# Kernel tuning notes

Hardware: AMD Instinct MI355X
Metric: run time of the kernel (lower is better)

Reference implementation:

```python
import jax, jax.numpy as jnp
import numpy as np

V, D = 100000, 128
B, Q, C, T = 1024, 64, 64, 8


def setup_inputs() -> dict:
    key = jax.random.key(0)
    ks = jax.random.split(key, 9)
    embed = jax.random.normal(ks[0], (V, D), dtype=jnp.float32) * 0.1
    embed = embed.at[0].set(0.0)  # padding_idx=0
    q_ids = jax.random.randint(ks[1], (B, Q), 1, V)
    c_ids = jax.random.randint(ks[2], (B, C, T), 1, V)
    num_qs = jax.random.randint(ks[3], (B,), 1, Q + 1)
    num_cols = jax.random.randint(ks[4], (B,), 1, C + 1)
    W_h = jax.random.normal(ks[5], (5 * D, D), dtype=jnp.float32) * 0.02
    b_h = jnp.zeros((D,), jnp.float32)
    W_o = jax.random.normal(ks[6], (D, 1), dtype=jnp.float32) * 0.02
    b_o = jnp.zeros((1,), jnp.float32)
    return {"q_ids": q_ids, "c_ids": c_ids, "num_qs": num_qs, "num_cols": num_cols,
            "embed": embed, "W_h": W_h, "b_h": b_h, "W_o": W_o, "b_o": b_o}


def _forward(q_ids, c_ids, num_qs, num_cols, embed, W_h, b_h, W_o, b_o):
    d = embed.shape[1]
    # ColumnSummarizer: pad-masked mean over column tokens -> [B, C, D]
    c_tok = embed[c_ids]                       # [B, C, T, D]
    c_mask = (c_ids != 0).astype(c_tok.dtype)  # [B, C, T]
    denom = jnp.maximum(c_mask.sum(-1, keepdims=True), 1.0)
    c_h = (c_tok * c_mask[..., None]).sum(-2) / denom  # [B, C, D]
    # QuestionSummarizer: q_h = token embeddings, q_summary = length-masked mean
    q_h = embed[q_ids]                         # [B, Q, D]
    q_valid = (jnp.arange(q_h.shape[1])[None, :] < num_qs[:, None])  # [B, Q]
    qv = q_valid.astype(q_h.dtype)
    q_summary = (q_h * qv[..., None]).sum(1) / jnp.maximum(
        num_qs[:, None].astype(q_h.dtype), 1.0)  # [B, D]
    # scaled dot-product attention, columns attend over question tokens
    sim = jnp.einsum('bcd,bqd->bcq', c_h, q_h) / jnp.sqrt(jnp.asarray(d, c_h.dtype))
    sim = jnp.where(q_valid[:, None, :], sim, -jnp.inf)  # mask padded q tokens
    att = jax.nn.softmax(sim, axis=-1)                    # [B, C, Q]
    weighted_q = jnp.einsum('bcq,bqd->bcd', att, q_h)     # [B, C, D]
    q_tiled = jnp.broadcast_to(q_summary[:, None, :], c_h.shape)
    feats = jnp.concatenate(
        [q_tiled, c_h, weighted_q, c_h * weighted_q, jnp.abs(c_h - weighted_q)],
        axis=-1)                                           # [B, C, 5D]
    h = jnp.tanh(feats @ W_h + b_h)
    return h @ W_o + b_o                                   # [B, C, 1]


def reference(q_ids, c_ids, num_qs, num_cols, embed, W_h, b_h, W_o, b_o):
    return _forward(q_ids, c_ids, num_qs, num_cols, embed, W_h, b_h, W_o, b_o)
```

## Files before the change

### kernel.cpp

```cpp
#include <hip/hip_runtime.h>


typedef __attribute__((ext_vector_type(8))) short     short8;
typedef __attribute__((ext_vector_type(8))) __bf16    bf16x8;
typedef __attribute__((ext_vector_type(4))) float     f32x4;

#define SWZ(row, off) ((off) ^ (((row) & 7) << 4))

#define CH_OFF    0
#define QH_OFF    16384
#define QHT_OFF   32768
#define ATT_OFF   49152
#define PROD_OFF  57344
#define QPART_OFF 73728
#define QSUM_OFF  77824
#define OUTP_OFF  78080
#define LDS_SIZE  79104

__device__ __forceinline__ unsigned short f2bf(float x) {
    unsigned u = __builtin_bit_cast(unsigned, x);
    u += 0x7FFFu + ((u >> 16) & 1u);
    return (unsigned short)(u >> 16);
}
__device__ __forceinline__ float bf2f(unsigned short u) {
    return __builtin_bit_cast(float, ((unsigned)u) << 16);
}
__device__ __forceinline__ f32x4 mfma16(short8 a, short8 b, f32x4 c) {
    return __builtin_amdgcn_mfma_f32_16x16x32_bf16(
        __builtin_bit_cast(bf16x8, a), __builtin_bit_cast(bf16x8, b), c, 0, 0, 0);
}

__global__ __launch_bounds__(256) void el_prep(const float* __restrict__ W_h,
                                               unsigned short* __restrict__ whT) {
    int t = blockIdx.x * 256 + threadIdx.x;
    int k = t >> 7, n = t & 127;
    whT[n * 640 + k] = f2bf(W_h[t]);
}

__global__ __launch_bounds__(256) void el_main(
    const int* __restrict__ q_ids, const int* __restrict__ c_ids,
    const int* __restrict__ num_qs, const float* __restrict__ embed,
    const unsigned short* __restrict__ whT, const float* __restrict__ b_h,
    const float* __restrict__ W_o, const float* __restrict__ b_o,
    float* __restrict__ out)
{
    __shared__ __align__(16) char smem[LDS_SIZE];
    const int tid = threadIdx.x;
    const int b = blockIdx.x;
    const int nq = num_qs[b];

    {
        const int l = tid & 31, g = tid >> 5;
        for (int c = g; c < 64; c += 8) {
            const int* cid = c_ids + ((b << 6) + c) * 8;
            f32x4 acc = {0.f, 0.f, 0.f, 0.f};
            int cnt = 0;
            #pragma unroll
            for (int t = 0; t < 8; ++t) {
                int id = cid[t];
                cnt += (id != 0);
                f32x4 v = *(const f32x4*)(embed + (long)id * 128 + l * 4);
                acc += v;
            }
            float inv = 1.0f / (float)(cnt > 0 ? cnt : 1);
            unsigned u01 = (unsigned)f2bf(acc[0] * inv) | ((unsigned)f2bf(acc[1] * inv) << 16);
            unsigned u23 = (unsigned)f2bf(acc[2] * inv) | ((unsigned)f2bf(acc[3] * inv) << 16);
            uint2 pk; pk.x = u01; pk.y = u23;
            *(uint2*)(smem + CH_OFF + SWZ(c, c * 256 + l * 8)) = pk;
        }
        f32x4 qacc = {0.f, 0.f, 0.f, 0.f};
        for (int q = g; q < 64; q += 8) {
            int id = q_ids[(b << 6) + q];
            f32x4 v = *(const f32x4*)(embed + (long)id * 128 + l * 4);
            unsigned u01 = (unsigned)f2bf(v[0]) | ((unsigned)f2bf(v[1]) << 16);
            unsigned u23 = (unsigned)f2bf(v[2]) | ((unsigned)f2bf(v[3]) << 16);
            uint2 pk; pk.x = u01; pk.y = u23;
            *(uint2*)(smem + QH_OFF + SWZ(q, q * 256 + l * 8)) = pk;
            #pragma unroll
            for (int i = 0; i < 4; ++i) {
                int d = l * 4 + i;
                *(unsigned short*)(smem + QHT_OFF + SWZ(d, d * 128 + q * 2)) = f2bf(v[i]);
            }
            if (q < nq) qacc += v;
        }
        *(f32x4*)(smem + QPART_OFF + (g * 128 + l * 4) * 4) = qacc;
    }
    __syncthreads();

    if (tid < 128) {
        float s = 0.f;
        #pragma unroll
        for (int g = 0; g < 8; ++g)
            s += *(const float*)(smem + QPART_OFF + (g * 128 + tid) * 4);
        s /= (float)(nq > 0 ? nq : 1);
        *(unsigned short*)(smem + QSUM_OFF + tid * 2) = f2bf(s);
    }
    __syncthreads();

    const int lane = tid & 63, w = tid >> 6;
    const int lr = lane & 15, lg = lane >> 4;

    {
        short8 a[4];
        const int arow = w * 16 + lr;
        #pragma unroll
        for (int s = 0; s < 4; ++s)
            a[s] = *(const short8*)(smem + CH_OFF + SWZ(arow, arow * 256 + s * 64 + lg * 16));
        f32x4 sim[4];
        #pragma unroll
        for (int ct = 0; ct < 4; ++ct) {
            f32x4 acc = {0.f, 0.f, 0.f, 0.f};
            const int q = ct * 16 + lr;
            #pragma unroll
            for (int s = 0; s < 4; ++s) {
                short8 bf = *(const short8*)(smem + QH_OFF + SWZ(q, q * 256 + s * 64 + lg * 16));
                acc = mfma16(a[s], bf, acc);
            }
            sim[ct] = acc;
        }
        const float scale = 0.08838834764831845f;
        #pragma unroll
        for (int ct = 0; ct < 4; ++ct) {
            const int q = ct * 16 + lr;
            #pragma unroll
            for (int r = 0; r < 4; ++r)
                sim[ct][r] = (q < nq) ? sim[ct][r] * scale : -3.0e38f;
        }
        float mx[4], sm[4];
        #pragma unroll
        for (int r = 0; r < 4; ++r)
            mx[r] = fmaxf(fmaxf(sim[0][r], sim[1][r]), fmaxf(sim[2][r], sim[3][r]));
        #pragma unroll
        for (int off = 1; off <= 8; off <<= 1)
            #pragma unroll
            for (int r = 0; r < 4; ++r)
                mx[r] = fmaxf(mx[r], __shfl_xor(mx[r], off));
        #pragma unroll
        for (int ct = 0; ct < 4; ++ct)
            #pragma unroll
            for (int r = 0; r < 4; ++r)
                sim[ct][r] = __expf(sim[ct][r] - mx[r]);
        #pragma unroll
        for (int r = 0; r < 4; ++r)
            sm[r] = (sim[0][r] + sim[1][r]) + (sim[2][r] + sim[3][r]);
        #pragma unroll
        for (int off = 1; off <= 8; off <<= 1)
            #pragma unroll
            for (int r = 0; r < 4; ++r)
                sm[r] += __shfl_xor(sm[r], off);
        float inv[4];
        #pragma unroll
        for (int r = 0; r < 4; ++r) inv[r] = 1.0f / sm[r];
        const int cbase = w * 16 + lg * 4;
        #pragma unroll
        for (int ct = 0; ct < 4; ++ct)
            #pragma unroll
            for (int r = 0; r < 4; ++r) {
                int c = cbase + r, q = ct * 16 + lr;
                *(unsigned short*)(smem + ATT_OFF + SWZ(c, c * 128 + q * 2)) =
                    f2bf(sim[ct][r] * inv[r]);
            }
    }
    __syncthreads();

    f32x4 wqa[8];
    {
        short8 pa[2];
        const int prow = w * 16 + lr;
        #pragma unroll
        for (int s = 0; s < 2; ++s)
            pa[s] = *(const short8*)(smem + ATT_OFF + SWZ(prow, prow * 128 + s * 64 + lg * 16));
        #pragma unroll
        for (int ct = 0; ct < 8; ++ct) {
            f32x4 acc = {0.f, 0.f, 0.f, 0.f};
            const int dcol = ct * 16 + lr;
            #pragma unroll
            for (int s = 0; s < 2; ++s) {
                short8 bf = *(const short8*)(smem + QHT_OFF + SWZ(dcol, dcol * 128 + s * 64 + lg * 16));
                acc = mfma16(pa[s], bf, acc);
            }
            wqa[ct] = acc;
        }
    }
    __syncthreads();
    {
        const int cbase = w * 16 + lg * 4;
        #pragma unroll
        for (int ct = 0; ct < 8; ++ct)
            #pragma unroll
            for (int r = 0; r < 4; ++r) {
                int c = cbase + r, d = ct * 16 + lr;
                int off = c * 256 + d * 2;
                float wqv = wqa[ct][r];
                float chv = bf2f(*(const unsigned short*)(smem + CH_OFF + SWZ(c, off)));
                *(unsigned short*)(smem + QH_OFF  + SWZ(c, off)) = f2bf(wqv);
                *(unsigned short*)(smem + PROD_OFF + SWZ(c, off)) = f2bf(chv * wqv);
                *(unsigned short*)(smem + QHT_OFF + SWZ(c, off)) = f2bf(fabsf(chv - wqv));
            }
    }
    __syncthreads();

    {
        f32x4 acc[4][2];
        #pragma unroll
        for (int rt = 0; rt < 4; ++rt)
            #pragma unroll
            for (int j = 0; j < 2; ++j)
                acc[rt][j] = (f32x4){0.f, 0.f, 0.f, 0.f};

        const int n0 = (w * 2) * 16 + lr;
        const int n1 = (w * 2 + 1) * 16 + lr;
        const int klane = lg * 8;
        short8 b0 = *(const short8*)(whT + n0 * 640 + klane);
        short8 b1 = *(const short8*)(whT + n1 * 640 + klane);

        for (int s = 0; s < 20; ++s) {
            short8 nb0 = b0, nb1 = b1;
            if (s < 19) {
                nb0 = *(const short8*)(whT + n0 * 640 + (s + 1) * 32 + klane);
                nb1 = *(const short8*)(whT + n1 * 640 + (s + 1) * 32 + klane);
            }
            const int p = s >> 2, sk = (s & 3) * 32;
            if (p == 0) {
                short8 afr = *(const short8*)(smem + QSUM_OFF + sk * 2 + lg * 16);
                #pragma unroll
                for (int rt = 0; rt < 4; ++rt) {
                    acc[rt][0] = mfma16(afr, b0, acc[rt][0]);
                    acc[rt][1] = mfma16(afr, b1, acc[rt][1]);
                }
            } else {
                const int base = (p == 1) ? CH_OFF : (p == 2) ? QH_OFF
                               : (p == 3) ? PROD_OFF : QHT_OFF;
                #pragma unroll
                for (int rt = 0; rt < 4; ++rt) {
                    int row = rt * 16 + lr;
                    short8 afr = *(const short8*)(smem + base + SWZ(row, row * 256 + sk * 2 + lg * 16));
                    acc[rt][0] = mfma16(afr, b0, acc[rt][0]);
                    acc[rt][1] = mfma16(afr, b1, acc[rt][1]);
                }
            }
            b0 = nb0; b1 = nb1;
        }

        float bh0 = b_h[n0], bh1 = b_h[n1];
        float wo0 = W_o[n0], wo1 = W_o[n1];
        #pragma unroll
        for (int rt = 0; rt < 4; ++rt)
            #pragma unroll
            for (int r = 0; r < 4; ++r) {
                float x0 = acc[rt][0][r] + bh0;
                float x1 = acc[rt][1][r] + bh1;
                float t0 = 1.0f - 2.0f / (__expf(2.0f * x0) + 1.0f);
                float t1 = 1.0f - 2.0f / (__expf(2.0f * x1) + 1.0f);
                float po = t0 * wo0 + t1 * wo1;
                #pragma unroll
                for (int off = 1; off <= 8; off <<= 1)
                    po += __shfl_xor(po, off);
                if (lr == 0)
                    *(float*)(smem + OUTP_OFF + (w * 64 + rt * 16 + lg * 4 + r) * 4) = po;
            }
    }
    __syncthreads();

    if (tid < 64) {
        float o = b_o[0];
        #pragma unroll
        for (int w2 = 0; w2 < 4; ++w2)
            o += *(const float*)(smem + OUTP_OFF + (w2 * 64 + tid) * 4);
        out[(b << 6) + tid] = o;
    }
}

extern "C" void kernel_launch(void* const* d_in, const int* in_sizes, int n_in,
                              void* d_out, int out_size, void* d_ws, size_t ws_size,
                              hipStream_t stream) {
    const int*   q_ids  = (const int*)d_in[0];
    const int*   c_ids  = (const int*)d_in[1];
    const int*   num_qs = (const int*)d_in[2];
    const float* embed  = (const float*)d_in[4];
    const float* W_h    = (const float*)d_in[5];
    const float* b_h    = (const float*)d_in[6];
    const float* W_o    = (const float*)d_in[7];
    const float* b_o    = (const float*)d_in[8];
    float*       out    = (float*)d_out;
    unsigned short* whT = (unsigned short*)d_ws;

    el_prep<<<320, 256, 0, stream>>>(W_h, whT);
    el_main<<<1024, 256, 0, stream>>>(q_ids, c_ids, num_qs, embed, whT,
                                      b_h, W_o, b_o, out);
}
```

Before: 171.3 us.

## Gather from a bf16 embedding copy, shrink LDS, fuse feature products into GEMM

Each call now converts the whole embedding table to bf16 in a separate pass, and the main kernel gathers column and question tokens from that copy. This halves the bytes moved by the random row gathers, at the cost of a full-table read and write per call. The LDS layout is compacted and buffers are reused so more blocks can fit per CU, and the launch bound now asks for three. The product and absolute-difference features are computed in registers inside the hidden-layer MFMA loop instead of being stored to LDS. The question transpose and the question summary are rebuilt from LDS, and token ids are staged in shared memory first.

```diff
diff --git a/kernel.cpp b/kernel.cpp
--- a/kernel.cpp
+++ b/kernel.cpp
@@ -10,12 +10,13 @@
 #define CH_OFF    0
 #define QH_OFF    16384
 #define QHT_OFF   32768
-#define ATT_OFF   49152
-#define PROD_OFF  57344
-#define QPART_OFF 73728
-#define QSUM_OFF  77824
-#define OUTP_OFF  78080
-#define LDS_SIZE  79104
+#define X_OFF     49152
+#define IDS_C     (X_OFF)
+#define IDS_Q     (X_OFF + 2048)
+#define QSP_OFF   (X_OFF)
+#define QSUM_OFF  (X_OFF + 1024)
+#define OUTP_OFF  (X_OFF + 1280)
+#define LDS_SIZE  (X_OFF + 2304)
 
 __device__ __forceinline__ unsigned short f2bf(float x) {
     unsigned u = __builtin_bit_cast(unsigned, x);
@@ -24,6 +25,12 @@
 }
 __device__ __forceinline__ float bf2f(unsigned short u) {
     return __builtin_bit_cast(float, ((unsigned)u) << 16);
+}
+__device__ __forceinline__ float bflo(unsigned u) {
+    return __builtin_bit_cast(float, u << 16);
+}
+__device__ __forceinline__ float bfhi(unsigned u) {
+    return __builtin_bit_cast(float, u & 0xFFFF0000u);
 }
 __device__ __forceinline__ f32x4 mfma16(short8 a, short8 b, f32x4 c) {
     return __builtin_amdgcn_mfma_f32_16x16x32_bf16(
@@ -37,9 +44,24 @@
     whT[n * 640 + k] = f2bf(W_h[t]);
 }
 
-__global__ __launch_bounds__(256) void el_main(
+__global__ __launch_bounds__(256) void el_conv(const float* __restrict__ e,
+                                               unsigned short* __restrict__ ebf) {
+    long i = ((long)blockIdx.x * 256 + threadIdx.x) * 8;
+    f32x4 a = *(const f32x4*)(e + i);
+    f32x4 c = *(const f32x4*)(e + i + 4);
+    uint4 pk;
+    pk.x = (unsigned)f2bf(a[0]) | ((unsigned)f2bf(a[1]) << 16);
+    pk.y = (unsigned)f2bf(a[2]) | ((unsigned)f2bf(a[3]) << 16);
+    pk.z = (unsigned)f2bf(c[0]) | ((unsigned)f2bf(c[1]) << 16);
+    pk.w = (unsigned)f2bf(c[2]) | ((unsigned)f2bf(c[3]) << 16);
+    *(uint4*)(ebf + i) = pk;
+}
+
+template <bool BF16E>
+__global__ __launch_bounds__(256, 3) void el_main(
     const int* __restrict__ q_ids, const int* __restrict__ c_ids,
-    const int* __restrict__ num_qs, const float* __restrict__ embed,
+    const int* __restrict__ num_qs, const float* __restrict__ emb,
+    const unsigned short* __restrict__ ebf,
     const unsigned short* __restrict__ whT, const float* __restrict__ b_h,
     const float* __restrict__ W_o, const float* __restrict__ b_o,
     float* __restrict__ out)
@@ -47,59 +69,120 @@
     __shared__ __align__(16) char smem[LDS_SIZE];
     const int tid = threadIdx.x;
     const int b = blockIdx.x;
-    const int nq = num_qs[b];
-
-    {
+    const int nq = num_qs[b] > 0 ? num_qs[b] : 1;
+
+    {
+        int* idc = (int*)(smem + IDS_C);
+        idc[tid]       = c_ids[(b << 9) + tid];
+        idc[tid + 256] = c_ids[(b << 9) + tid + 256];
+        if (tid < 64) ((int*)(smem + IDS_Q))[tid] = q_ids[(b << 6) + tid];
+    }
+    __syncthreads();
+
+    if constexpr (BF16E) {
+        const int l4 = tid & 15, gg = tid >> 4;
+        #pragma unroll 2
+        for (int cc = 0; cc < 4; ++cc) {
+            const int c = gg + cc * 16;
+            const int* idp = (const int*)(smem + IDS_C) + c * 8;
+            int id8[8];
+            #pragma unroll
+            for (int t = 0; t < 8; ++t) id8[t] = idp[t];
+            float acc[8] = {0.f,0.f,0.f,0.f,0.f,0.f,0.f,0.f};
+            int cnt = 0;
+            #pragma unroll
+            for (int t = 0; t < 8; ++t) {
+                uint4 v = *(const uint4*)(ebf + (long)id8[t] * 128 + l4 * 8);
+                cnt += (id8[t] != 0);
+                acc[0] += bflo(v.x); acc[1] += bfhi(v.x);
+                acc[2] += bflo(v.y); acc[3] += bfhi(v.y);
+                acc[4] += bflo(v.z); acc[5] += bfhi(v.z);
+                acc[6] += bflo(v.w); acc[7] += bfhi(v.w);
+            }
+            float inv = 1.0f / (float)(cnt > 0 ? cnt : 1);
+            uint4 pk;
+            pk.x = (unsigned)f2bf(acc[0]*inv) | ((unsigned)f2bf(acc[1]*inv) << 16);
+            pk.y = (unsigned)f2bf(acc[2]*inv) | ((unsigned)f2bf(acc[3]*inv) << 16);
+            pk.z = (unsigned)f2bf(acc[4]*inv) | ((unsigned)f2bf(acc[5]*inv) << 16);
+            pk.w = (unsigned)f2bf(acc[6]*inv) | ((unsigned)f2bf(acc[7]*inv) << 16);
+            *(uint4*)(smem + CH_OFF + SWZ(c, c * 256 + l4 * 16)) = pk;
+        }
+        #pragma unroll
+        for (int qq = 0; qq < 4; ++qq) {
+            const int q = gg + qq * 16;
+            int id = ((const int*)(smem + IDS_Q))[q];
+            uint4 v = *(const uint4*)(ebf + (long)id * 128 + l4 * 8);
+            *(uint4*)(smem + QH_OFF + SWZ(q, q * 256 + l4 * 16)) = v;
+        }
+    } else {
         const int l = tid & 31, g = tid >> 5;
-        for (int c = g; c < 64; c += 8) {
-            const int* cid = c_ids + ((b << 6) + c) * 8;
+        #pragma unroll 2
+        for (int cc = 0; cc < 8; ++cc) {
+            const int c = g + cc * 8;
+            const int* idp = (const int*)(smem + IDS_C) + c * 8;
+            int id8[8];
+            #pragma unroll
+            for (int t = 0; t < 8; ++t) id8[t] = idp[t];
             f32x4 acc = {0.f, 0.f, 0.f, 0.f};
             int cnt = 0;
             #pragma unroll
             for (int t = 0; t < 8; ++t) {
-                int id = cid[t];
-                cnt += (id != 0);
-                f32x4 v = *(const f32x4*)(embed + (long)id * 128 + l * 4);
+                f32x4 v = *(const f32x4*)(emb + (long)id8[t] * 128 + l * 4);
+                cnt += (id8[t] != 0);
                 acc += v;
             }
             float inv = 1.0f / (float)(cnt > 0 ? cnt : 1);
-            unsigned u01 = (unsigned)f2bf(acc[0] * inv) | ((unsigned)f2bf(acc[1] * inv) << 16);
-            unsigned u23 = (unsigned)f2bf(acc[2] * inv) | ((unsigned)f2bf(acc[3] * inv) << 16);
-            uint2 pk; pk.x = u01; pk.y = u23;
+            uint2 pk;
+            pk.x = (unsigned)f2bf(acc[0]*inv) | ((unsigned)f2bf(acc[1]*inv) << 16);
+            pk.y = (unsigned)f2bf(acc[2]*inv) | ((unsigned)f2bf(acc[3]*inv) << 16);
             *(uint2*)(smem + CH_OFF + SWZ(c, c * 256 + l * 8)) = pk;
         }
-        f32x4 qacc = {0.f, 0.f, 0.f, 0.f};
-        for (int q = g; q < 64; q += 8) {
-            int id = q_ids[(b << 6) + q];
-            f32x4 v = *(const f32x4*)(embed + (long)id * 128 + l * 4);
-            unsigned u01 = (unsigned)f2bf(v[0]) | ((unsigned)f2bf(v[1]) << 16);
-            unsigned u23 = (unsigned)f2bf(v[2]) | ((unsigned)f2bf(v[3]) << 16);
-            uint2 pk; pk.x = u01; pk.y = u23;
+        #pragma unroll
+        for (int qq = 0; qq < 8; ++qq) {
+            const int q = g + qq * 8;
+            int id = ((const int*)(smem + IDS_Q))[q];
+            f32x4 v = *(const f32x4*)(emb + (long)id * 128 + l * 4);
+            uint2 pk;
+            pk.x = (unsigned)f2bf(v[0]) | ((unsigned)f2bf(v[1]) << 16);
+            pk.y = (unsigned)f2bf(v[2]) | ((unsigned)f2bf(v[3]) << 16);
             *(uint2*)(smem + QH_OFF + SWZ(q, q * 256 + l * 8)) = pk;
-            #pragma unroll
-            for (int i = 0; i < 4; ++i) {
-                int d = l * 4 + i;
-                *(unsigned short*)(smem + QHT_OFF + SWZ(d, d * 128 + q * 2)) = f2bf(v[i]);
-            }
-            if (q < nq) qacc += v;
-        }
-        *(f32x4*)(smem + QPART_OFF + (g * 128 + l * 4) * 4) = qacc;
-    }
-    __syncthreads();
-
-    if (tid < 128) {
+        }
+    }
+    __syncthreads();
+
+    {
+        const int d = tid >> 1, qh = (tid & 1) * 32;
+        unsigned v16[32];
+        #pragma unroll
+        for (int j = 0; j < 32; ++j) {
+            int q = qh + j;
+            v16[j] = *(const unsigned short*)(smem + QH_OFF + SWZ(q, q * 256 + d * 2));
+        }
+        #pragma unroll
+        for (int i = 0; i < 4; ++i) {
+            uint4 pk;
+            pk.x = v16[i*8+0] | (v16[i*8+1] << 16);
+            pk.y = v16[i*8+2] | (v16[i*8+3] << 16);
+            pk.z = v16[i*8+4] | (v16[i*8+5] << 16);
+            pk.w = v16[i*8+6] | (v16[i*8+7] << 16);
+            *(uint4*)(smem + QHT_OFF + SWZ(d, d * 128 + qh * 2 + i * 16)) = pk;
+        }
+        const int d2 = tid & 127, h = tid >> 7;
         float s = 0.f;
         #pragma unroll
-        for (int g = 0; g < 8; ++g)
-            s += *(const float*)(smem + QPART_OFF + (g * 128 + tid) * 4);
-        s /= (float)(nq > 0 ? nq : 1);
-        *(unsigned short*)(smem + QSUM_OFF + tid * 2) = f2bf(s);
+        for (int j = 0; j < 32; ++j) {
+            int q = h * 32 + j;
+            float v = bf2f(*(const unsigned short*)(smem + QH_OFF + SWZ(q, q * 256 + d2 * 2)));
+            s += (q < nq) ? v : 0.f;
+        }
+        ((float*)(smem + QSP_OFF))[h * 128 + d2] = s;
     }
     __syncthreads();
 
     const int lane = tid & 63, w = tid >> 6;
     const int lr = lane & 15, lg = lane >> 4;
 
+    float attv[4][4];
     {
         short8 a[4];
         const int arow = w * 16 + lr;
@@ -148,18 +231,28 @@
             #pragma unroll
             for (int r = 0; r < 4; ++r)
                 sm[r] += __shfl_xor(sm[r], off);
-        float inv[4];
-        #pragma unroll
-        for (int r = 0; r < 4; ++r) inv[r] = 1.0f / sm[r];
+        #pragma unroll
+        for (int ct = 0; ct < 4; ++ct)
+            #pragma unroll
+            for (int r = 0; r < 4; ++r)
+                attv[ct][r] = sim[ct][r] * (1.0f / sm[r]);
+    }
+    __syncthreads();
+    {
         const int cbase = w * 16 + lg * 4;
         #pragma unroll
         for (int ct = 0; ct < 4; ++ct)
             #pragma unroll
             for (int r = 0; r < 4; ++r) {
                 int c = cbase + r, q = ct * 16 + lr;
-                *(unsigned short*)(smem + ATT_OFF + SWZ(c, c * 128 + q * 2)) =
-                    f2bf(sim[ct][r] * inv[r]);
-            }
+                *(unsigned short*)(smem + QH_OFF + SWZ(c, c * 128 + q * 2)) =
+                    f2bf(attv[ct][r]);
+            }
+        if (tid < 128) {
+            const float* qsp = (const float*)(smem + QSP_OFF);
+            float s = (qsp[tid] + qsp[128 + tid]) / (float)nq;
+            *(unsigned short*)(smem + QSUM_OFF + tid * 2) = f2bf(s);
+        }
     }
     __syncthreads();
 
@@ -169,7 +262,7 @@
         const int prow = w * 16 + lr;
         #pragma unroll
         for (int s = 0; s < 2; ++s)
-            pa[s] = *(const short8*)(smem + ATT_OFF + SWZ(prow, prow * 128 + s * 64 + lg * 16));
+            pa[s] = *(const short8*)(smem + QH_OFF + SWZ(prow, prow * 128 + s * 64 + lg * 16));
         #pragma unroll
         for (int ct = 0; ct < 8; ++ct) {
             f32x4 acc = {0.f, 0.f, 0.f, 0.f};
@@ -190,12 +283,7 @@
             #pragma unroll
             for (int r = 0; r < 4; ++r) {
                 int c = cbase + r, d = ct * 16 + lr;
-                int off = c * 256 + d * 2;
-                float wqv = wqa[ct][r];
-                float chv = bf2f(*(const unsigned short*)(smem + CH_OFF + SWZ(c, off)));
-                *(unsigned short*)(smem + QH_OFF  + SWZ(c, off)) = f2bf(wqv);
-                *(unsigned short*)(smem + PROD_OFF + SWZ(c, off)) = f2bf(chv * wqv);
-                *(unsigned short*)(smem + QHT_OFF + SWZ(c, off)) = f2bf(fabsf(chv - wqv));
+                *(unsigned short*)(smem + QH_OFF + SWZ(c, c * 256 + d * 2)) = f2bf(wqa[ct][r]);
             }
     }
     __syncthreads();
@@ -203,43 +291,44 @@
     {
         f32x4 acc[4][2];
         #pragma unroll
-        for (int rt = 0; rt < 4; ++rt)
-            #pragma unroll
-            for (int j = 0; j < 2; ++j)
-                acc[rt][j] = (f32x4){0.f, 0.f, 0.f, 0.f};
-
-        const int n0 = (w * 2) * 16 + lr;
-        const int n1 = (w * 2 + 1) * 16 + lr;
-        const int klane = lg * 8;
-        short8 b0 = *(const short8*)(whT + n0 * 640 + klane);
-        short8 b1 = *(const short8*)(whT + n1 * 640 + klane);
-
-        for (int s = 0; s < 20; ++s) {
-            short8 nb0 = b0, nb1 = b1;
-            if (s < 19) {
-                nb0 = *(const short8*)(whT + n0 * 640 + (s + 1) * 32 + klane);
-                nb1 = *(const short8*)(whT + n1 * 640 + (s + 1) * 32 + klane);
-            }
-            const int p = s >> 2, sk = (s & 3) * 32;
-            if (p == 0) {
-                short8 afr = *(const short8*)(smem + QSUM_OFF + sk * 2 + lg * 16);
+        for (int rt = 0; rt < 4; ++rt) {
+            acc[rt][0] = (f32x4){0.f, 0.f, 0.f, 0.f};
+            acc[rt][1] = (f32x4){0.f, 0.f, 0.f, 0.f};
+        }
+        const int n0 = w * 32 + lr, n1 = n0 + 16;
+
+        for (int sk = 0; sk < 4; ++sk) {
+            short8 B0[5], B1[5];
+            #pragma unroll
+            for (int p = 0; p < 5; ++p) {
+                B0[p] = *(const short8*)(whT + n0 * 640 + p * 128 + sk * 32 + lg * 8);
+                B1[p] = *(const short8*)(whT + n1 * 640 + p * 128 + sk * 32 + lg * 8);
+            }
+            short8 qsf = *(const short8*)(smem + QSUM_OFF + sk * 64 + lg * 16);
+            #pragma unroll
+            for (int rt = 0; rt < 4; ++rt) {
+                const int row = rt * 16 + lr;
+                short8 chf = *(const short8*)(smem + CH_OFF + SWZ(row, row * 256 + sk * 64 + lg * 16));
+                short8 wqf = *(const short8*)(smem + QH_OFF + SWZ(row, row * 256 + sk * 64 + lg * 16));
+                short8 prf, adf;
                 #pragma unroll
-                for (int rt = 0; rt < 4; ++rt) {
-                    acc[rt][0] = mfma16(afr, b0, acc[rt][0]);
-                    acc[rt][1] = mfma16(afr, b1, acc[rt][1]);
+                for (int e = 0; e < 8; ++e) {
+                    float cv = bf2f((unsigned short)chf[e]);
+                    float wv = bf2f((unsigned short)wqf[e]);
+                    prf[e] = (short)f2bf(cv * wv);
+                    adf[e] = (short)f2bf(fabsf(cv - wv));
                 }
-            } else {
-                const int base = (p == 1) ? CH_OFF : (p == 2) ? QH_OFF
-                               : (p == 3) ? PROD_OFF : QHT_OFF;
-                #pragma unroll
-                for (int rt = 0; rt < 4; ++rt) {
-                    int row = rt * 16 + lr;
-                    short8 afr = *(const short8*)(smem + base + SWZ(row, row * 256 + sk * 2 + lg * 16));
-                    acc[rt][0] = mfma16(afr, b0, acc[rt][0]);
-                    acc[rt][1] = mfma16(afr, b1, acc[rt][1]);
-                }
-            }
-            b0 = nb0; b1 = nb1;
+                acc[rt][0] = mfma16(qsf, B0[0], acc[rt][0]);
+                acc[rt][1] = mfma16(qsf, B1[0], acc[rt][1]);
+                acc[rt][0] = mfma16(chf, B0[1], acc[rt][0]);
+                acc[rt][1] = mfma16(chf, B1[1], acc[rt][1]);
+                acc[rt][0] = mfma16(wqf, B0[2], acc[rt][0]);
+                acc[rt][1] = mfma16(wqf, B1[2], acc[rt][1]);
+                acc[rt][0] = mfma16(prf, B0[3], acc[rt][0]);
+                acc[rt][1] = mfma16(prf, B1[3], acc[rt][1]);
+                acc[rt][0] = mfma16(adf, B0[4], acc[rt][0]);
+                acc[rt][1] = mfma16(adf, B1[4], acc[rt][1]);
+            }
         }
 
         float bh0 = b_h[n0], bh1 = b_h[n1];
@@ -283,9 +372,19 @@
     const float* W_o    = (const float*)d_in[7];
     const float* b_o    = (const float*)d_in[8];
     float*       out    = (float*)d_out;
+
     unsigned short* whT = (unsigned short*)d_ws;
+    unsigned short* ebf = (unsigned short*)d_ws + 81920;
 
     el_prep<<<320, 256, 0, stream>>>(W_h, whT);
-    el_main<<<1024, 256, 0, stream>>>(q_ids, c_ids, num_qs, embed, whT,
-                                      b_h, W_o, b_o, out);
-}
+
+    const bool bf16e = ws_size >= (size_t)(163840 + 100000 * 128 * 2);
+    if (bf16e) {
+        el_conv<<<6250, 256, 0, stream>>>(embed, ebf);
+        el_main<true><<<1024, 256, 0, stream>>>(q_ids, c_ids, num_qs, embed, ebf,
+                                                whT, b_h, W_o, b_o, out);
+    } else {
+        el_main<false><<<1024, 256, 0, stream>>>(q_ids, c_ids, num_qs, embed, ebf,
+                                                 whT, b_h, W_o, b_o, out);
+    }
+}
```

Result: faster. 158.6 us (-7.4%).
